# Kernel tuning notes

Hardware: AMD Instinct MI355X
Metric: run time of the kernel (lower is better)

Reference implementation:

```python
import jax, jax.numpy as jnp
import numpy as np

N_NODES = 100000
N_EDGES = 1600000
IN_DIM = 128
HID_DIM = 256
LN_EPS = 1e-5


def setup_inputs() -> dict:
    key = jax.random.key(0)
    ks = jax.random.split(key, 5)
    features = jax.random.normal(ks[0], (N_NODES, IN_DIM), dtype=jnp.float32)
    src = jax.random.randint(ks[1], (N_EDGES,), 0, N_NODES, dtype=jnp.int64)
    dst = jax.random.randint(ks[2], (N_EDGES,), 0, N_NODES, dtype=jnp.int64)
    W = jax.random.normal(ks[3], (IN_DIM, HID_DIM), dtype=jnp.float32) / np.sqrt(IN_DIM)
    b = jnp.zeros((HID_DIM,), dtype=jnp.float32)
    gamma = jnp.ones((HID_DIM,), dtype=jnp.float32)
    beta = jnp.zeros((HID_DIM,), dtype=jnp.float32)
    skip_W = jax.random.normal(ks[4], (IN_DIM, HID_DIM), dtype=jnp.float32) / np.sqrt(IN_DIM)
    skip_b = jnp.zeros((HID_DIM,), dtype=jnp.float32)
    return {"features": features, "src": src, "dst": dst, "W": W, "b": b,
            "gamma": gamma, "beta": beta, "skip_W": skip_W, "skip_b": skip_b}


def reference(features, src, dst, W, b, gamma, beta, skip_W, skip_b):
    N = features.shape[0]
    ones_e = jnp.ones(src.shape[0], dtype=features.dtype)
    # DGL GraphConv norm='both': symmetric degree normalization, degrees clamped to >= 1
    deg_out = jax.ops.segment_sum(ones_e, src, num_segments=N)
    deg_in = jax.ops.segment_sum(ones_e, dst, num_segments=N)
    norm_src = jax.lax.rsqrt(jnp.maximum(deg_out, 1.0))  # [N]
    norm_dst = jax.lax.rsqrt(jnp.maximum(deg_in, 1.0))   # [N]
    h = features * norm_src[:, None]                      # [N, F_in]
    agg = jax.ops.segment_sum(h[src], dst, num_segments=N)  # SpMM: [N, F_in]
    agg = agg * norm_dst[:, None]
    gcn = agg @ W + b                                     # [N, F_out]
    # LayerNorm over feature dim
    mu = jnp.mean(gcn, axis=-1, keepdims=True)
    var = jnp.mean(jnp.square(gcn - mu), axis=-1, keepdims=True)
    ln = (gcn - mu) * jax.lax.rsqrt(var + LN_EPS) * gamma + beta
    # ReLU activation, dropout=0 (identity), skip linear projection
    return jax.nn.relu(ln) + (features @ skip_W + skip_b)
```

## Files before the change

kernel.cpp:

```cpp
#include <hip/hip_runtime.h>
#include <hip/hip_bf16.h>

#define N_NODES 100000
#define N_EDGES 1600000
#define IN_DIM 128
#define HID_DIM 256
#define LN_EPS 1e-5f
#define NT32 (N_NODES / 32)

#define NCHUNK 32
#define CHUNK_E (N_EDGES / NCHUNK)
#define NSLICE 8
#define SLICE (N_NODES / NSLICE)
#define HBLK (NCHUNK * NSLICE)

#define EDGE_BLOCKS (N_EDGES / 256)
#define FCVT_BLOCKS (N_NODES * 32 / 256)

typedef short bf16x8 __attribute__((ext_vector_type(8)));
typedef float f32x4  __attribute__((ext_vector_type(4)));

static __device__ __forceinline__ short f2bf(float x) {
    return __builtin_bit_cast(short, __float2bfloat16(x));
}
static __device__ __forceinline__ float bf2f_lo(unsigned v) {
    return __builtin_bit_cast(float, v << 16);
}
static __device__ __forceinline__ float bf2f_hi(unsigned v) {
    return __builtin_bit_cast(float, v & 0xffff0000u);
}

__global__ __launch_bounds__(1024)
void hist_kernel(const int* __restrict__ src, const int* __restrict__ dst,
                 unsigned* __restrict__ p_out, unsigned* __restrict__ p_in,
                 ushort* __restrict__ rank16) {
    __shared__ unsigned bins[SLICE];
    const int b = blockIdx.x;
    const bool isdst = (b >= HBLK);
    const int bb = isdst ? (b - HBLK) : b;
    const int ci = bb >> 3;
    const int si = bb & 7;
    const int s0 = si * SLICE;

    for (int i = threadIdx.x; i < SLICE; i += 1024) bins[i] = 0;
    __syncthreads();

    const int4* ep4 = (const int4*)((isdst ? dst : src) + ci * CHUNK_E);
    if (isdst) {
        const int ebase = ci * CHUNK_E;
        for (int i = threadIdx.x; i < CHUNK_E / 4; i += 1024) {
            int4 v = ep4[i];
            int e0 = ebase + i * 4;
            unsigned u0 = (unsigned)(v.x - s0);
            unsigned u1 = (unsigned)(v.y - s0);
            unsigned u2 = (unsigned)(v.z - s0);
            unsigned u3 = (unsigned)(v.w - s0);
            if (u0 < SLICE) rank16[e0 + 0] = (ushort)atomicAdd(&bins[u0], 1u);
            if (u1 < SLICE) rank16[e0 + 1] = (ushort)atomicAdd(&bins[u1], 1u);
            if (u2 < SLICE) rank16[e0 + 2] = (ushort)atomicAdd(&bins[u2], 1u);
            if (u3 < SLICE) rank16[e0 + 3] = (ushort)atomicAdd(&bins[u3], 1u);
        }
    } else {
        for (int i = threadIdx.x; i < CHUNK_E / 4; i += 1024) {
            int4 v = ep4[i];
            unsigned u0 = (unsigned)(v.x - s0);
            unsigned u1 = (unsigned)(v.y - s0);
            unsigned u2 = (unsigned)(v.z - s0);
            unsigned u3 = (unsigned)(v.w - s0);
            if (u0 < SLICE) atomicAdd(&bins[u0], 1u);
            if (u1 < SLICE) atomicAdd(&bins[u1], 1u);
            if (u2 < SLICE) atomicAdd(&bins[u2], 1u);
            if (u3 < SLICE) atomicAdd(&bins[u3], 1u);
        }
    }
    __syncthreads();

    unsigned* pp = (isdst ? p_in : p_out) + (size_t)ci * N_NODES + s0;
    for (int i = threadIdx.x; i < SLICE; i += 1024) pp[i] = bins[i];
}

__global__ __launch_bounds__(256)
void prefix_kernel(const unsigned* __restrict__ p_out, unsigned* __restrict__ p_in,
                   float* __restrict__ nsrc, unsigned* __restrict__ deg_in) {
    int n = blockIdx.x * 256 + threadIdx.x;
    if (n >= N_NODES) return;
    unsigned so = 0;
    #pragma unroll
    for (int c = 0; c < NCHUNK; ++c) so += p_out[(size_t)c * N_NODES + n];
    nsrc[n] = rsqrtf(fmaxf((float)so, 1.f));
    unsigned run = 0;
    #pragma unroll
    for (int c = 0; c < NCHUNK; ++c) {
        unsigned t = p_in[(size_t)c * N_NODES + n];
        p_in[(size_t)c * N_NODES + n] = run;
        run += t;
    }
    deg_in[n] = run;
}

__global__ void wcvt_kernel(const float* __restrict__ W, const float* __restrict__ sW,
                            const float* __restrict__ bvec, const float* __restrict__ gamma,
                            const float* __restrict__ beta, const float* __restrict__ skipb,
                            ushort* __restrict__ Wfrag, ushort* __restrict__ sWfrag,
                            float4* __restrict__ params) {
    int tid = blockIdx.x * blockDim.x + threadIdx.x;
    if (tid >= 8448) return;
    if (tid >= 8192) {
        int i = tid - 8192;
        params[i] = make_float4(bvec[i], gamma[i], beta[i], skipb[i]);
        return;
    }
    const float* srcm = (tid < 4096) ? W : sW;
    ushort* dstm = (tid < 4096) ? Wfrag : sWfrag;
    int u = tid & 4095;
    int lane = u & 63;
    int ks = (u >> 6) & 3;
    int n = u >> 8;
    int c = lane & 15, g = lane >> 4;
    int col = n * 16 + c;
    int k0 = ks * 32 + g * 8;
    ushort4 lo, hi;
    lo.x = (ushort)f2bf(srcm[(size_t)(k0 + 0) * HID_DIM + col]);
    lo.y = (ushort)f2bf(srcm[(size_t)(k0 + 1) * HID_DIM + col]);
    lo.z = (ushort)f2bf(srcm[(size_t)(k0 + 2) * HID_DIM + col]);
    lo.w = (ushort)f2bf(srcm[(size_t)(k0 + 3) * HID_DIM + col]);
    hi.x = (ushort)f2bf(srcm[(size_t)(k0 + 4) * HID_DIM + col]);
    hi.y = (ushort)f2bf(srcm[(size_t)(k0 + 5) * HID_DIM + col]);
    hi.z = (ushort)f2bf(srcm[(size_t)(k0 + 6) * HID_DIM + col]);
    hi.w = (ushort)f2bf(srcm[(size_t)(k0 + 7) * HID_DIM + col]);
    *(ushort4*)(dstm + (size_t)u * 8)     = lo;
    *(ushort4*)(dstm + (size_t)u * 8 + 4) = hi;
}

__global__ __launch_bounds__(1024)
void scan_kernel(const unsigned* __restrict__ deg_in, unsigned* __restrict__ row_ptr) {
    __shared__ unsigned wsum[16];
    __shared__ unsigned carry_s;
    if (threadIdx.x == 0) carry_s = 0;
    __syncthreads();
    const int lane = threadIdx.x & 63;
    const int wid  = threadIdx.x >> 6;
    for (int base = 0; base < N_NODES; base += 4096) {
        int i0 = base + threadIdx.x * 4;
        unsigned d0 = 0, d1 = 0, d2 = 0, d3 = 0;
        if (i0 < N_NODES) {
            uint4 v = *(const uint4*)(deg_in + i0);
            d0 = v.x; d1 = v.y; d2 = v.z; d3 = v.w;
        }
        unsigned t = d0 + d1 + d2 + d3;
        unsigned x = t;
        #pragma unroll
        for (int d = 1; d < 64; d <<= 1) {
            unsigned tt = __shfl_up(x, d, 64);
            if (lane >= d) x += tt;
        }
        if (lane == 63) wsum[wid] = x;
        __syncthreads();
        if (threadIdx.x == 0) {
            unsigned run = carry_s;
            #pragma unroll
            for (int w = 0; w < 16; ++w) { unsigned tmp = wsum[w]; wsum[w] = run; run += tmp; }
            carry_s = run;
        }
        __syncthreads();
        if (i0 < N_NODES) {
            unsigned b = wsum[wid] + (x - t);
            uint4 rp;
            rp.x = b; rp.y = b + d0; rp.z = b + d0 + d1; rp.w = b + d0 + d1 + d2;
            *(uint4*)(row_ptr + i0) = rp;
        }
        __syncthreads();
    }
    if (threadIdx.x == 0) row_ptr[N_NODES] = carry_s;
}

__global__ __launch_bounds__(256)
void pre2_kernel(const int* __restrict__ src, const int* __restrict__ dst,
                 const unsigned* __restrict__ row_ptr, const unsigned* __restrict__ p_in,
                 const ushort* __restrict__ rank16, unsigned* __restrict__ edge_src,
                 const float* __restrict__ feat, ushort* __restrict__ featb) {
    const int b = blockIdx.x;
    if (b < EDGE_BLOCKS) {
        int e = b * 256 + threadIdx.x;
        int d = dst[e];
        int c = e / CHUNK_E;
        unsigned pos = row_ptr[d] + p_in[(size_t)c * N_NODES + d] + (unsigned)rank16[e];
        edge_src[pos] = (unsigned)src[e];
    } else {
        int id = (b - EDGE_BLOCKS) * 256 + threadIdx.x;
        float4 v = ((const float4*)feat)[id];
        ushort4 o;
        o.x = (ushort)f2bf(v.x);
        o.y = (ushort)f2bf(v.y);
        o.z = (ushort)f2bf(v.z);
        o.w = (ushort)f2bf(v.w);
        ((ushort4*)featb)[id] = o;
    }
}

__global__ __launch_bounds__(256)
void spmm_kernel(const ushort* __restrict__ featb, const float* __restrict__ nsrc,
                 const unsigned* __restrict__ row_ptr, const unsigned* __restrict__ edge_src,
                 unsigned* __restrict__ aggb_u32) {
    int gw = (blockIdx.x * 256 + threadIdx.x) >> 6;
    int lane = threadIdx.x & 63;
    if (gw >= N_NODES) return;
    unsigned beg = row_ptr[gw], end = row_ptr[gw + 1];
    float a0 = 0.f, a1 = 0.f;
    unsigned e = beg;
    for (; e + 8 <= end; e += 8) {
        unsigned s[8];
        #pragma unroll
        for (int q = 0; q < 8; ++q) s[q] = edge_src[e + q];
        float ns[8];
        #pragma unroll
        for (int q = 0; q < 8; ++q) ns[q] = nsrc[s[q]];
        unsigned v[8];
        #pragma unroll
        for (int q = 0; q < 8; ++q)
            v[q] = *(const unsigned*)(featb + (size_t)s[q] * IN_DIM + 2 * lane);
        #pragma unroll
        for (int q = 0; q < 8; ++q) {
            a0 = fmaf(bf2f_lo(v[q]), ns[q], a0);
            a1 = fmaf(bf2f_hi(v[q]), ns[q], a1);
        }
    }
    for (; e < end; ++e) {
        unsigned s = edge_src[e];
        float ns = nsrc[s];
        unsigned v = *(const unsigned*)(featb + (size_t)s * IN_DIM + 2 * lane);
        a0 = fmaf(bf2f_lo(v), ns, a0); a1 = fmaf(bf2f_hi(v), ns, a1);
    }
    float nd = rsqrtf(fmaxf((float)(end - beg), 1.0f));
    unsigned lo = (unsigned)(ushort)f2bf(a0 * nd);
    unsigned hi = (unsigned)(ushort)f2bf(a1 * nd);
    aggb_u32[(size_t)gw * (IN_DIM / 2) + lane] = lo | (hi << 16);
}

__global__ __launch_bounds__(256)
void gemm_fused_kernel(const ushort* __restrict__ aggb, const ushort* __restrict__ featb,
                       const ushort* __restrict__ Wfrag, const ushort* __restrict__ sWfrag,
                       const float4* __restrict__ params, float* __restrict__ out) {
    __shared__ float2 red[4][32];
    const int tid = threadIdx.x;
    const int lane = tid & 63;
    const int h = tid >> 6;
    const int c = lane & 15, g = lane >> 4;
    const int r0 = blockIdx.x * 32;
    const int n0 = h * 4;

    bf16x8 A[2][4];
    #pragma unroll
    for (int rg = 0; rg < 2; ++rg)
        #pragma unroll
        for (int ks = 0; ks < 4; ++ks)
            A[rg][ks] = *(const bf16x8*)(aggb + (size_t)(r0 + rg * 16 + c) * IN_DIM
                                         + ks * 32 + g * 8);

    f32x4 acc[2][4];
    #pragma unroll
    for (int i = 0; i < 4; ++i) {
        float bb = params[(n0 + i) * 16 + c].x;
        acc[0][i] = (f32x4){bb, bb, bb, bb};
        acc[1][i] = (f32x4){bb, bb, bb, bb};
        #pragma unroll
        for (int ks = 0; ks < 4; ++ks) {
            bf16x8 b = *(const bf16x8*)(Wfrag + (((n0 + i) * 4 + ks) * 64 + lane) * 8);
            acc[0][i] = __builtin_amdgcn_mfma_f32_16x16x32_bf16(A[0][ks], b, acc[0][i], 0, 0, 0);
            acc[1][i] = __builtin_amdgcn_mfma_f32_16x16x32_bf16(A[1][ks], b, acc[1][i], 0, 0, 0);
        }
    }

    #pragma unroll
    for (int rg = 0; rg < 2; ++rg)
        #pragma unroll
        for (int ks = 0; ks < 4; ++ks)
            A[rg][ks] = *(const bf16x8*)(featb + (size_t)(r0 + rg * 16 + c) * IN_DIM
                                         + ks * 32 + g * 8);

    {
        float s1[2][4], s2[2][4];
        #pragma unroll
        for (int rg = 0; rg < 2; ++rg)
            #pragma unroll
            for (int j = 0; j < 4; ++j) { s1[rg][j] = 0.f; s2[rg][j] = 0.f; }
        #pragma unroll
        for (int rg = 0; rg < 2; ++rg)
            #pragma unroll
            for (int i = 0; i < 4; ++i)
                #pragma unroll
                for (int j = 0; j < 4; ++j) {
                    s1[rg][j] += acc[rg][i][j];
                    s2[rg][j] = fmaf(acc[rg][i][j], acc[rg][i][j], s2[rg][j]);
                }
        #pragma unroll
        for (int m = 1; m <= 8; m <<= 1)
            #pragma unroll
            for (int rg = 0; rg < 2; ++rg)
                #pragma unroll
                for (int j = 0; j < 4; ++j) {
                    s1[rg][j] += __shfl_xor(s1[rg][j], m, 64);
                    s2[rg][j] += __shfl_xor(s2[rg][j], m, 64);
                }
        if (c == 0) {
            #pragma unroll
            for (int rg = 0; rg < 2; ++rg)
                #pragma unroll
                for (int j = 0; j < 4; ++j)
                    red[h][rg * 16 + g * 4 + j] = make_float2(s1[rg][j], s2[rg][j]);
        }
    }
    __syncthreads();

    float mu[2][4], rstd[2][4];
    #pragma unroll
    for (int rg = 0; rg < 2; ++rg)
        #pragma unroll
        for (int j = 0; j < 4; ++j) {
            int row = rg * 16 + g * 4 + j;
            float2 p0 = red[0][row];
            float2 p1 = red[1][row];
            float2 p2 = red[2][row];
            float2 p3 = red[3][row];
            float t1 = (p0.x + p1.x) + (p2.x + p3.x);
            float t2 = (p0.y + p1.y) + (p2.y + p3.y);
            mu[rg][j] = t1 * (1.f / HID_DIM);
            float var = t2 * (1.f / HID_DIM) - mu[rg][j] * mu[rg][j];
            rstd[rg][j] = rsqrtf(var + LN_EPS);
        }

    #pragma unroll
    for (int i = 0; i < 4; ++i) {
        float4 p = params[(n0 + i) * 16 + c];
        #pragma unroll
        for (int rg = 0; rg < 2; ++rg)
            #pragma unroll
            for (int j = 0; j < 4; ++j)
                acc[rg][i][j] = fmaxf(fmaf((acc[rg][i][j] - mu[rg][j]) * rstd[rg][j],
                                           p.y, p.z), 0.f) + p.w;
    }

    #pragma unroll
    for (int i = 0; i < 4; ++i) {
        #pragma unroll
        for (int ks = 0; ks < 4; ++ks) {
            bf16x8 b = *(const bf16x8*)(sWfrag + (((n0 + i) * 4 + ks) * 64 + lane) * 8);
            acc[0][i] = __builtin_amdgcn_mfma_f32_16x16x32_bf16(A[0][ks], b, acc[0][i], 0, 0, 0);
            acc[1][i] = __builtin_amdgcn_mfma_f32_16x16x32_bf16(A[1][ks], b, acc[1][i], 0, 0, 0);
        }
    }

    #pragma unroll
    for (int rg = 0; rg < 2; ++rg)
        #pragma unroll
        for (int i = 0; i < 4; ++i)
            #pragma unroll
            for (int j = 0; j < 4; ++j)
                out[(size_t)(r0 + rg * 16 + g * 4 + j) * HID_DIM + (n0 + i) * 16 + c]
                    = acc[rg][i][j];
}

extern "C" void kernel_launch(void* const* d_in, const int* in_sizes, int n_in,
                              void* d_out, int out_size, void* d_ws, size_t ws_size,
                              hipStream_t stream) {
    const float* feat  = (const float*)d_in[0];
    const int*   src   = (const int*)d_in[1];
    const int*   dst   = (const int*)d_in[2];
    const float* W     = (const float*)d_in[3];
    const float* bvec  = (const float*)d_in[4];
    const float* gamma = (const float*)d_in[5];
    const float* beta  = (const float*)d_in[6];
    const float* skipW = (const float*)d_in[7];
    const float* skipb = (const float*)d_in[8];
    float* out = (float*)d_out;

    char* ws = (char*)d_ws;
    ushort*   Wfrag    = (ushort*)ws;
    ushort*   sWfrag   = Wfrag + 32768;
    float4*   params   = (float4*)(sWfrag + 32768);
    ushort*   aggb     = (ushort*)(params + 256);
    char*     xbase    = (char*)(aggb + (size_t)N_NODES * IN_DIM);
    ushort*   featb    = (ushort*)xbase;
    unsigned* p_out    = (unsigned*)xbase;
    unsigned* edge_src = (unsigned*)(featb + (size_t)N_NODES * IN_DIM);
    ushort*   rank16   = (ushort*)(edge_src + N_EDGES);
    unsigned* p_in     = (unsigned*)(rank16 + N_EDGES);
    float*    nsrc     = (float*)(p_in + (size_t)NCHUNK * N_NODES);
    unsigned* deg_in   = (unsigned*)(nsrc + N_NODES);
    unsigned* row_ptr  = deg_in + N_NODES;

    wcvt_kernel<<<33, 256, 0, stream>>>(W, skipW, bvec, gamma, beta, skipb,
                                        Wfrag, sWfrag, params);

    hist_kernel<<<2 * HBLK, 1024, 0, stream>>>(src, dst, p_out, p_in, rank16);

    prefix_kernel<<<(N_NODES + 255) / 256, 256, 0, stream>>>(p_out, p_in, nsrc, deg_in);

    scan_kernel<<<1, 1024, 0, stream>>>(deg_in, row_ptr);

    pre2_kernel<<<EDGE_BLOCKS + FCVT_BLOCKS, 256, 0, stream>>>(
        src, dst, row_ptr, p_in, rank16, edge_src, feat, featb);

    spmm_kernel<<<(N_NODES * 64 + 255) / 256, 256, 0, stream>>>(featb, nsrc, row_ptr,
                                                                edge_src, (unsigned*)aggb);

    gemm_fused_kernel<<<NT32, 256, 0, stream>>>(
        aggb, featb, Wfrag, sWfrag, params, out);
}
```

Before: 237.7 us.

## Pack histogram bins as 16-bit pairs and halve slice count

Histogram bins now pack two 16-bit counters into each 32-bit shared word, so each block covers twice as many nodes. The number of node slices drops from 8 to 4, which halves the redundant edge-chunk reads. Per-chunk counts and in-chunk offsets are stored as ushort, which halves the global traffic in the prefix and scatter kernels. It also adds a min-blocks hint to the fused GEMM launch bounds. This relies on per-chunk per-node counts staying below 65536, and packed atomics may raise shared-memory contention.

Measured after the change: 218.0 us. 1.09x faster.

```diff
diff --git a/kernel.cpp b/kernel.cpp
--- a/kernel.cpp
+++ b/kernel.cpp
@@ -10,8 +10,9 @@
 
 #define NCHUNK 32
 #define CHUNK_E (N_EDGES / NCHUNK)
-#define NSLICE 8
+#define NSLICE 4
 #define SLICE (N_NODES / NSLICE)
+#define SLICE_W (SLICE / 2)
 #define HBLK (NCHUNK * NSLICE)
 
 #define EDGE_BLOCKS (N_EDGES / 256)
@@ -32,17 +33,17 @@
 
 __global__ __launch_bounds__(1024)
 void hist_kernel(const int* __restrict__ src, const int* __restrict__ dst,
-                 unsigned* __restrict__ p_out, unsigned* __restrict__ p_in,
+                 ushort* __restrict__ p_out16, ushort* __restrict__ p_in16,
                  ushort* __restrict__ rank16) {
-    __shared__ unsigned bins[SLICE];
+    __shared__ unsigned bins[SLICE_W];
     const int b = blockIdx.x;
     const bool isdst = (b >= HBLK);
     const int bb = isdst ? (b - HBLK) : b;
-    const int ci = bb >> 3;
-    const int si = bb & 7;
+    const int ci = bb >> 2;
+    const int si = bb & 3;
     const int s0 = si * SLICE;
 
-    for (int i = threadIdx.x; i < SLICE; i += 1024) bins[i] = 0;
+    for (int i = threadIdx.x; i < SLICE_W; i += 1024) bins[i] = 0;
     __syncthreads();
 
     const int4* ep4 = (const int4*)((isdst ? dst : src) + ci * CHUNK_E);
@@ -55,10 +56,22 @@
             unsigned u1 = (unsigned)(v.y - s0);
             unsigned u2 = (unsigned)(v.z - s0);
             unsigned u3 = (unsigned)(v.w - s0);
-            if (u0 < SLICE) rank16[e0 + 0] = (ushort)atomicAdd(&bins[u0], 1u);
-            if (u1 < SLICE) rank16[e0 + 1] = (ushort)atomicAdd(&bins[u1], 1u);
-            if (u2 < SLICE) rank16[e0 + 2] = (ushort)atomicAdd(&bins[u2], 1u);
-            if (u3 < SLICE) rank16[e0 + 3] = (ushort)atomicAdd(&bins[u3], 1u);
+            if (u0 < SLICE) {
+                unsigned sh = (u0 & 1) * 16;
+                rank16[e0 + 0] = (ushort)(atomicAdd(&bins[u0 >> 1], 1u << sh) >> sh);
+            }
+            if (u1 < SLICE) {
+                unsigned sh = (u1 & 1) * 16;
+                rank16[e0 + 1] = (ushort)(atomicAdd(&bins[u1 >> 1], 1u << sh) >> sh);
+            }
+            if (u2 < SLICE) {
+                unsigned sh = (u2 & 1) * 16;
+                rank16[e0 + 2] = (ushort)(atomicAdd(&bins[u2 >> 1], 1u << sh) >> sh);
+            }
+            if (u3 < SLICE) {
+                unsigned sh = (u3 & 1) * 16;
+                rank16[e0 + 3] = (ushort)(atomicAdd(&bins[u3 >> 1], 1u << sh) >> sh);
+            }
         }
     } else {
         for (int i = threadIdx.x; i < CHUNK_E / 4; i += 1024) {
@@ -67,32 +80,32 @@
             unsigned u1 = (unsigned)(v.y - s0);
             unsigned u2 = (unsigned)(v.z - s0);
             unsigned u3 = (unsigned)(v.w - s0);
-            if (u0 < SLICE) atomicAdd(&bins[u0], 1u);
-            if (u1 < SLICE) atomicAdd(&bins[u1], 1u);
-            if (u2 < SLICE) atomicAdd(&bins[u2], 1u);
-            if (u3 < SLICE) atomicAdd(&bins[u3], 1u);
+            if (u0 < SLICE) atomicAdd(&bins[u0 >> 1], 1u << ((u0 & 1) * 16));
+            if (u1 < SLICE) atomicAdd(&bins[u1 >> 1], 1u << ((u1 & 1) * 16));
+            if (u2 < SLICE) atomicAdd(&bins[u2 >> 1], 1u << ((u2 & 1) * 16));
+            if (u3 < SLICE) atomicAdd(&bins[u3 >> 1], 1u << ((u3 & 1) * 16));
         }
     }
     __syncthreads();
 
-    unsigned* pp = (isdst ? p_in : p_out) + (size_t)ci * N_NODES + s0;
-    for (int i = threadIdx.x; i < SLICE; i += 1024) pp[i] = bins[i];
+    unsigned* pp = (unsigned*)((isdst ? p_in16 : p_out16) + (size_t)ci * N_NODES + s0);
+    for (int i = threadIdx.x; i < SLICE_W; i += 1024) pp[i] = bins[i];
 }
 
 __global__ __launch_bounds__(256)
-void prefix_kernel(const unsigned* __restrict__ p_out, unsigned* __restrict__ p_in,
+void prefix_kernel(const ushort* __restrict__ p_out16, ushort* __restrict__ p_in16,
                    float* __restrict__ nsrc, unsigned* __restrict__ deg_in) {
     int n = blockIdx.x * 256 + threadIdx.x;
     if (n >= N_NODES) return;
     unsigned so = 0;
     #pragma unroll
-    for (int c = 0; c < NCHUNK; ++c) so += p_out[(size_t)c * N_NODES + n];
+    for (int c = 0; c < NCHUNK; ++c) so += p_out16[(size_t)c * N_NODES + n];
     nsrc[n] = rsqrtf(fmaxf((float)so, 1.f));
     unsigned run = 0;
     #pragma unroll
     for (int c = 0; c < NCHUNK; ++c) {
-        unsigned t = p_in[(size_t)c * N_NODES + n];
-        p_in[(size_t)c * N_NODES + n] = run;
+        unsigned t = p_in16[(size_t)c * N_NODES + n];
+        p_in16[(size_t)c * N_NODES + n] = (ushort)run;
         run += t;
     }
     deg_in[n] = run;
@@ -176,7 +189,7 @@
 
 __global__ __launch_bounds__(256)
 void pre2_kernel(const int* __restrict__ src, const int* __restrict__ dst,
-                 const unsigned* __restrict__ row_ptr, const unsigned* __restrict__ p_in,
+                 const unsigned* __restrict__ row_ptr, const ushort* __restrict__ p_in16,
                  const ushort* __restrict__ rank16, unsigned* __restrict__ edge_src,
                  const float* __restrict__ feat, ushort* __restrict__ featb) {
     const int b = blockIdx.x;
@@ -184,7 +197,8 @@
         int e = b * 256 + threadIdx.x;
         int d = dst[e];
         int c = e / CHUNK_E;
-        unsigned pos = row_ptr[d] + p_in[(size_t)c * N_NODES + d] + (unsigned)rank16[e];
+        unsigned pos = row_ptr[d] + (unsigned)p_in16[(size_t)c * N_NODES + d]
+                     + (unsigned)rank16[e];
         edge_src[pos] = (unsigned)src[e];
     } else {
         int id = (b - EDGE_BLOCKS) * 256 + threadIdx.x;
@@ -237,7 +251,7 @@
     aggb_u32[(size_t)gw * (IN_DIM / 2) + lane] = lo | (hi << 16);
 }
 
-__global__ __launch_bounds__(256)
+__global__ __launch_bounds__(256, 4)
 void gemm_fused_kernel(const ushort* __restrict__ aggb, const ushort* __restrict__ featb,
                        const ushort* __restrict__ Wfrag, const ushort* __restrict__ sWfrag,
                        const float4* __restrict__ params, float* __restrict__ out) {
@@ -381,25 +395,25 @@
     ushort*   aggb     = (ushort*)(params + 256);
     char*     xbase    = (char*)(aggb + (size_t)N_NODES * IN_DIM);
     ushort*   featb    = (ushort*)xbase;
-    unsigned* p_out    = (unsigned*)xbase;
+    ushort*   p_out16  = (ushort*)xbase;
     unsigned* edge_src = (unsigned*)(featb + (size_t)N_NODES * IN_DIM);
     ushort*   rank16   = (ushort*)(edge_src + N_EDGES);
-    unsigned* p_in     = (unsigned*)(rank16 + N_EDGES);
-    float*    nsrc     = (float*)(p_in + (size_t)NCHUNK * N_NODES);
+    ushort*   p_in16   = rank16 + N_EDGES;
+    float*    nsrc     = (float*)(p_in16 + (size_t)NCHUNK * N_NODES);
     unsigned* deg_in   = (unsigned*)(nsrc + N_NODES);
     unsigned* row_ptr  = deg_in + N_NODES;
 
     wcvt_kernel<<<33, 256, 0, stream>>>(W, skipW, bvec, gamma, beta, skipb,
                                         Wfrag, sWfrag, params);
 
-    hist_kernel<<<2 * HBLK, 1024, 0, stream>>>(src, dst, p_out, p_in, rank16);
-
-    prefix_kernel<<<(N_NODES + 255) / 256, 256, 0, stream>>>(p_out, p_in, nsrc, deg_in);
+    hist_kernel<<<2 * HBLK, 1024, 0, stream>>>(src, dst, p_out16, p_in16, rank16);
+
+    prefix_kernel<<<(N_NODES + 255) / 256, 256, 0, stream>>>(p_out16, p_in16, nsrc, deg_in);
 
     scan_kernel<<<1, 1024, 0, stream>>>(deg_in, row_ptr);
 
     pre2_kernel<<<EDGE_BLOCKS + FCVT_BLOCKS, 256, 0, stream>>>(
-        src, dst, row_ptr, p_in, rank16, edge_src, feat, featb);
+        src, dst, row_ptr, p_in16, rank16, edge_src, feat, featb);
 
     spmm_kernel<<<(N_NODES * 64 + 255) / 256, 256, 0, stream>>>(featb, nsrc, row_ptr,
                                                                 edge_src, (unsigned*)aggb);
```
